# Kernel optimization log

Measured on AMD Instinct MI355X. Metric: run time of the kernel, lower is better.

Reference implementation:

```python
import jax, jax.numpy as jnp
import numpy as np

N_SRC = 50000
N_DST = 50000
N_EDGES = 1600000
BATCH = 64


def setup_inputs() -> dict:
    key = jax.random.key(0)
    k1, k2, k3, k4, k5 = jax.random.split(key, 5)
    x = jax.random.normal(k1, (BATCH, N_SRC), dtype=jnp.float32)
    # per-edge scalar weights, init like Synapse.init_weight: U(-v, v), v = sqrt(1/fan_in)~sqrt(1/32)
    v = float(np.sqrt(1.0 / 32.0))
    k = jax.random.uniform(k2, (N_EDGES,), dtype=jnp.float32, minval=-v, maxval=v)
    b = jax.random.normal(k3, (N_DST,), dtype=jnp.float32) * 0.1
    edge_src = jax.random.randint(k4, (N_EDGES,), 0, N_SRC, dtype=jnp.int32)
    edge_dst = jax.random.randint(k5, (N_EDGES,), 0, N_DST, dtype=jnp.int32)
    return {"x": x, "k": k, "b": b, "edge_src": edge_src, "edge_dst": edge_dst}


def reference(x, k, b, edge_src, edge_dst):
    # Synapse: out_e = k_e * source_output  (source output is x[:, src(e)], shape [batch])
    # msgs: [n_edges, batch]
    msgs = x.T[edge_src] * k[:, None]
    # DestinationNeuron: sum of dendrite outputs per destination + bias
    agg = jax.ops.segment_sum(msgs, edge_dst, num_segments=N_DST)  # [n_dst, batch]
    out = jax.nn.relu(agg.T + b[None, :])  # [batch, n_dst]
    return out
```

## Files before the change

### kernel.cpp

```cpp
#include <hip/hip_runtime.h>
#include <hip/hip_bf16.h>
#include <stdint.h>

#define N_SRC 50000
#define N_DST 50000
#define N_EDGES 1600000
#define BATCH 64

#define DPB 32
#define NBUCK ((N_DST + DPB - 1) / DPB)
#define CAPB 1344
#define EPB 6400
#define PTHREADS 1024
#define GTHREADS 512
#define NT ((EPB + PTHREADS - 1) / PTHREADS)

__global__ void transpose_kernel(const float* __restrict__ x,
                                 __hip_bfloat16* __restrict__ xTb,
                                 int* __restrict__ gcur) {
    __shared__ float tile[64][65];
    const int s0 = blockIdx.x * 64;
    const int tid = threadIdx.x;

    if (gcur && tid < 2) {
        const int i = blockIdx.x * 2 + tid;
        if (i < NBUCK) gcur[i] = 0;
    }

#pragma unroll
    for (int it = 0; it < 16; ++it) {
        const int i = it * 256 + tid;
        const int bi = i >> 6;
        const int sc = i & 63;
        const int s = s0 + sc;
        float v = 0.0f;
        if (s < N_SRC) v = x[(size_t)bi * N_SRC + s];
        tile[bi][sc] = v;
    }
    __syncthreads();
#pragma unroll
    for (int it = 0; it < 16; ++it) {
        const int i = it * 256 + tid;
        const int sc = i >> 6;
        const int bi = i & 63;
        const int s = s0 + sc;
        if (s < N_SRC) xTb[(size_t)s * 64 + bi] = __float2bfloat16(tile[bi][sc]);
    }
}

__global__ __launch_bounds__(PTHREADS) void partition_kernel(
        const float* __restrict__ k,
        const int* __restrict__ esrc,
        const int* __restrict__ edst,
        int* __restrict__ gcur,
        uint64_t* __restrict__ part) {
    __shared__ int bcnt[NBUCK];
    __shared__ int bcur[NBUCK];
    const int e0 = blockIdx.x * EPB;
    const int n = min(EPB, N_EDGES - e0);

    for (int i = threadIdx.x; i < NBUCK; i += PTHREADS) bcnt[i] = 0;
    __syncthreads();

    int dreg[NT];
#pragma unroll
    for (int t = 0; t < NT; ++t) {
        const int i = t * PTHREADS + threadIdx.x;
        dreg[t] = (i < n) ? edst[e0 + i] : -1;
        if (dreg[t] >= 0) atomicAdd(&bcnt[dreg[t] >> 5], 1);
    }
    __syncthreads();

    for (int bi = threadIdx.x; bi < NBUCK; bi += PTHREADS) {
        const int c = bcnt[bi];
        bcur[bi] = c ? atomicAdd(&gcur[bi], c) : 0;
    }
    __syncthreads();

#pragma unroll
    for (int t = 0; t < NT; ++t) {
        const int i = t * PTHREADS + threadIdx.x;
        if (dreg[t] >= 0) {
            const int e = e0 + i;
            const int d = dreg[t];
            const int bkt = d >> 5;
            const int slot = atomicAdd(&bcur[bkt], 1);
            if (slot < CAPB) {
                const uint32_t lo = (uint32_t)esrc[e] | ((uint32_t)(d & 31) << 16);
                part[(size_t)bkt * CAPB + slot] =
                    (uint64_t)lo | ((uint64_t)__float_as_uint(k[e]) << 32);
            }
        }
    }
}

__global__ __launch_bounds__(GTHREADS, 8) void gather_kernel(
        const __hip_bfloat16* __restrict__ xTb,
        const int* __restrict__ gcur,
        const uint64_t* __restrict__ part,
        const float* __restrict__ b,
        float* __restrict__ out) {
    __shared__ uint64_t raw[CAPB];
    __shared__ uint64_t sorted[CAPB];
    __shared__ int dbase[DPB + 1];
    __shared__ int dcur[DPB];

    const uint2* __restrict__ xTu2 = (const uint2*)xTb;

    const int bk = blockIdx.x;
    const size_t base = (size_t)bk * CAPB;
    const int n = min(gcur[bk], CAPB);
    const int d0 = bk * DPB;
    const int tid = threadIdx.x;
    const int wid = tid >> 6;
    const int lane = tid & 63;
    const int rp = lane >> 4;
    const int m = lane & 15;

    if (tid < DPB) dcur[tid] = 0;
    __syncthreads();

    for (int i = tid; i < n; i += GTHREADS) {
        const uint64_t r = part[base + i];
        raw[i] = r;
        atomicAdd(&dcur[(int)((r >> 16) & 31)], 1);
    }
    __syncthreads();

    if (wid == 0) {
        const int orig = (lane < DPB) ? dcur[lane] : 0;
        int v = orig;
#pragma unroll
        for (int d = 1; d < DPB; d <<= 1) {
            const int t = __shfl_up(v, d, 64);
            if (lane >= d) v += t;
        }
        if (lane < DPB) dbase[lane] = v - orig;
        if (lane == DPB - 1) dbase[DPB] = v;
    }
    __syncthreads();
    if (tid < DPB) dcur[tid] = dbase[tid];
    __syncthreads();

    for (int i = tid; i < n; i += GTHREADS) {
        const uint64_t r = raw[i];
        const int p = atomicAdd(&dcur[(int)((r >> 16) & 31)], 1);
        sorted[p] = r;
    }
    __syncthreads();

    float acc[4][4];
    const int dlo = wid * 4;
#pragma unroll
    for (int q = 0; q < 4; ++q) {
        const int dl = dlo + q;
        float a0 = 0.0f, a1 = 0.0f, a2 = 0.0f, a3 = 0.0f;
        int j = dbase[dl];
        const int je = dbase[dl + 1];
        for (; j + 8 <= je; j += 8) {
            const uint64_t r0 = sorted[j + rp];
            const uint64_t r1 = sorted[j + 4 + rp];
            const uint2 x0 = xTu2[(size_t)((uint32_t)r0 & 0xFFFFu) * 16 + m];
            const uint2 x1 = xTu2[(size_t)((uint32_t)r1 & 0xFFFFu) * 16 + m];
            const float k0 = __uint_as_float((uint32_t)(r0 >> 32));
            const float k1 = __uint_as_float((uint32_t)(r1 >> 32));
            a0 = fmaf(k0, __uint_as_float(x0.x << 16), a0);
            a1 = fmaf(k0, __uint_as_float(x0.x & 0xFFFF0000u), a1);
            a2 = fmaf(k0, __uint_as_float(x0.y << 16), a2);
            a3 = fmaf(k0, __uint_as_float(x0.y & 0xFFFF0000u), a3);
            a0 = fmaf(k1, __uint_as_float(x1.x << 16), a0);
            a1 = fmaf(k1, __uint_as_float(x1.x & 0xFFFF0000u), a1);
            a2 = fmaf(k1, __uint_as_float(x1.y << 16), a2);
            a3 = fmaf(k1, __uint_as_float(x1.y & 0xFFFF0000u), a3);
        }
        for (; j < je; j += 4) {
            const int idx = j + rp;
            const bool v = idx < je;
            const uint64_t r = sorted[v ? idx : j];
            const float kv = v ? __uint_as_float((uint32_t)(r >> 32)) : 0.0f;
            const uint2 xv = xTu2[(size_t)((uint32_t)r & 0xFFFFu) * 16 + m];
            a0 = fmaf(kv, __uint_as_float(xv.x << 16), a0);
            a1 = fmaf(kv, __uint_as_float(xv.x & 0xFFFF0000u), a1);
            a2 = fmaf(kv, __uint_as_float(xv.y << 16), a2);
            a3 = fmaf(kv, __uint_as_float(xv.y & 0xFFFF0000u), a3);
        }
        a0 += __shfl_xor(a0, 16); a0 += __shfl_xor(a0, 32);
        a1 += __shfl_xor(a1, 16); a1 += __shfl_xor(a1, 32);
        a2 += __shfl_xor(a2, 16); a2 += __shfl_xor(a2, 32);
        a3 += __shfl_xor(a3, 16); a3 += __shfl_xor(a3, 32);
        acc[q][0] = a0; acc[q][1] = a1; acc[q][2] = a2; acc[q][3] = a3;
    }
    __syncthreads();

    float* stg = (float*)sorted;
    if (rp == 0) {
#pragma unroll
        for (int q = 0; q < 4; ++q) {
            const int dl = dlo + q;
            stg[dl * 65 + 4 * m + 0] = acc[q][0];
            stg[dl * 65 + 4 * m + 1] = acc[q][1];
            stg[dl * 65 + 4 * m + 2] = acc[q][2];
            stg[dl * 65 + 4 * m + 3] = acc[q][3];
        }
    }
    __syncthreads();

    for (int i = tid; i < 64 * DPB; i += GTHREADS) {
        const int dl = i & (DPB - 1);
        const int bi = i >> 5;
        const int d = d0 + dl;
        if (d < N_DST)
            out[(size_t)bi * N_DST + d] = fmaxf(stg[dl * 65 + bi] + b[d], 0.0f);
    }
}

__global__ void scatter_kernel(const __hip_bfloat16* __restrict__ xTb,
                               const float* __restrict__ k,
                               const int* __restrict__ esrc,
                               const int* __restrict__ edst,
                               float* __restrict__ agg) {
    const int gtid = blockIdx.x * blockDim.x + threadIdx.x;
    const int wid = gtid >> 6;
    const int lane = threadIdx.x & 63;
    const int nwaves = (gridDim.x * blockDim.x) >> 6;
    for (int e = wid; e < N_EDGES; e += nwaves) {
        atomicAdd(&agg[(size_t)edst[e] * 64 + lane],
                  k[e] * __bfloat162float(xTb[(size_t)esrc[e] * 64 + lane]));
    }
}

__global__ void finish_kernel(const float* __restrict__ agg,
                              const float* __restrict__ b,
                              float* __restrict__ out) {
    __shared__ float tile[64 * 65];
    const int d0 = blockIdx.x * 64;
    const int tid = threadIdx.x;
#pragma unroll
    for (int it = 0; it < 16; ++it) {
        const int i = it * 256 + tid;
        const int dl = i >> 6;
        const int bi = i & 63;
        const int d = d0 + dl;
        float v = 0.0f;
        if (d < N_DST) v = agg[(size_t)d * 64 + bi];
        tile[bi * 65 + dl] = v;
    }
    __syncthreads();
#pragma unroll
    for (int it = 0; it < 16; ++it) {
        const int i = it * 256 + tid;
        const int bi = i >> 6;
        const int dl = i & 63;
        const int d = d0 + dl;
        if (d < N_DST)
            out[(size_t)bi * N_DST + d] = fmaxf(tile[bi * 65 + dl] + b[d], 0.0f);
    }
}

extern "C" void kernel_launch(void* const* d_in, const int* in_sizes, int n_in,
                              void* d_out, int out_size, void* d_ws, size_t ws_size,
                              hipStream_t stream) {
    const float* x    = (const float*)d_in[0];
    const float* k    = (const float*)d_in[1];
    const float* b    = (const float*)d_in[2];
    const int*   esrc = (const int*)d_in[3];
    const int*   edst = (const int*)d_in[4];
    float* out = (float*)d_out;

    const size_t xt_bytes   = (size_t)N_SRC * 64 * sizeof(__hip_bfloat16);
    const size_t part_bytes = (size_t)NBUCK * CAPB * sizeof(uint64_t);
    const size_t off_gcur   = xt_bytes + part_bytes;
    const size_t need_new   = off_gcur + ((NBUCK * 4 + 4095) & ~4095ull);

    __hip_bfloat16* xTb = (__hip_bfloat16*)d_ws;
    const int nblk_t = (N_SRC + 63) / 64;

    if (ws_size >= need_new) {
        uint64_t* part = (uint64_t*)((char*)d_ws + xt_bytes);
        int* gcur      = (int*)((char*)d_ws + off_gcur);

        transpose_kernel<<<nblk_t, 256, 0, stream>>>(x, xTb, gcur);
        const int nblk_p = (N_EDGES + EPB - 1) / EPB;
        partition_kernel<<<nblk_p, PTHREADS, 0, stream>>>(k, esrc, edst,
                                                          gcur, part);
        gather_kernel<<<NBUCK, GTHREADS, 0, stream>>>(xTb, gcur, part, b, out);
    } else {
        transpose_kernel<<<nblk_t, 256, 0, stream>>>(x, xTb, nullptr);
        float* agg = (float*)((char*)d_ws + ((xt_bytes + 255) & ~255ull));
        hipMemsetAsync(agg, 0, (size_t)N_DST * 64 * sizeof(float), stream);
        scatter_kernel<<<2048, 256, 0, stream>>>(xTb, k, esrc, edst, agg);
        const int nblk_f = (N_DST + 63) / 64;
        finish_kernel<<<nblk_f, 256, 0, stream>>>(agg, b, out);
    }
}
```

Measured before the change: 71.39 us.

## Fuse transpose and edge partition into one heterogeneous-block launch

Merges the x transpose and the edge bucket-partition kernels into a single launch where the first blocks partition edges and the remaining blocks transpose x to bf16. The gcur zeroing moves from the transpose kernel to a hipMemsetAsync before the launch. The aim is to overlap the two independent stages and drop one kernel boundary. In exchange, the transpose blocks now run at 1024 threads and carry the partition kernel's large shared-memory allocation, which may lower occupancy, and the added memset node brings its own overhead.

```diff
diff --git a/kernel.cpp b/kernel.cpp
--- a/kernel.cpp
+++ b/kernel.cpp
@@ -11,44 +11,15 @@
 #define NBUCK ((N_DST + DPB - 1) / DPB)
 #define CAPB 1344
 #define EPB 6400
+#define PBLOCKS ((N_EDGES + EPB - 1) / EPB)
+#define TBLOCKS ((N_SRC + 63) / 64)
 #define PTHREADS 1024
 #define GTHREADS 512
 #define NT ((EPB + PTHREADS - 1) / PTHREADS)
 
-__global__ void transpose_kernel(const float* __restrict__ x,
-                                 __hip_bfloat16* __restrict__ xTb,
-                                 int* __restrict__ gcur) {
-    __shared__ float tile[64][65];
-    const int s0 = blockIdx.x * 64;
-    const int tid = threadIdx.x;
-
-    if (gcur && tid < 2) {
-        const int i = blockIdx.x * 2 + tid;
-        if (i < NBUCK) gcur[i] = 0;
-    }
-
-#pragma unroll
-    for (int it = 0; it < 16; ++it) {
-        const int i = it * 256 + tid;
-        const int bi = i >> 6;
-        const int sc = i & 63;
-        const int s = s0 + sc;
-        float v = 0.0f;
-        if (s < N_SRC) v = x[(size_t)bi * N_SRC + s];
-        tile[bi][sc] = v;
-    }
-    __syncthreads();
-#pragma unroll
-    for (int it = 0; it < 16; ++it) {
-        const int i = it * 256 + tid;
-        const int sc = i >> 6;
-        const int bi = i & 63;
-        const int s = s0 + sc;
-        if (s < N_SRC) xTb[(size_t)s * 64 + bi] = __float2bfloat16(tile[bi][sc]);
-    }
-}
-
-__global__ __launch_bounds__(PTHREADS) void partition_kernel(
+__global__ __launch_bounds__(PTHREADS) void fused_tp_kernel(
+        const float* __restrict__ x,
+        __hip_bfloat16* __restrict__ xTb,
         const float* __restrict__ k,
         const int* __restrict__ esrc,
         const int* __restrict__ edst,
@@ -56,40 +27,69 @@
         uint64_t* __restrict__ part) {
     __shared__ int bcnt[NBUCK];
     __shared__ int bcur[NBUCK];
-    const int e0 = blockIdx.x * EPB;
-    const int n = min(EPB, N_EDGES - e0);
-
-    for (int i = threadIdx.x; i < NBUCK; i += PTHREADS) bcnt[i] = 0;
-    __syncthreads();
-
-    int dreg[NT];
-#pragma unroll
-    for (int t = 0; t < NT; ++t) {
-        const int i = t * PTHREADS + threadIdx.x;
-        dreg[t] = (i < n) ? edst[e0 + i] : -1;
-        if (dreg[t] >= 0) atomicAdd(&bcnt[dreg[t] >> 5], 1);
-    }
-    __syncthreads();
-
-    for (int bi = threadIdx.x; bi < NBUCK; bi += PTHREADS) {
-        const int c = bcnt[bi];
-        bcur[bi] = c ? atomicAdd(&gcur[bi], c) : 0;
-    }
-    __syncthreads();
-
-#pragma unroll
-    for (int t = 0; t < NT; ++t) {
-        const int i = t * PTHREADS + threadIdx.x;
-        if (dreg[t] >= 0) {
-            const int e = e0 + i;
-            const int d = dreg[t];
-            const int bkt = d >> 5;
-            const int slot = atomicAdd(&bcur[bkt], 1);
-            if (slot < CAPB) {
-                const uint32_t lo = (uint32_t)esrc[e] | ((uint32_t)(d & 31) << 16);
-                part[(size_t)bkt * CAPB + slot] =
-                    (uint64_t)lo | ((uint64_t)__float_as_uint(k[e]) << 32);
+    __shared__ float tile[64][65];
+
+    if (blockIdx.x < PBLOCKS) {
+        const int e0 = blockIdx.x * EPB;
+        const int n = min(EPB, N_EDGES - e0);
+
+        for (int i = threadIdx.x; i < NBUCK; i += PTHREADS) bcnt[i] = 0;
+        __syncthreads();
+
+        int dreg[NT];
+#pragma unroll
+        for (int t = 0; t < NT; ++t) {
+            const int i = t * PTHREADS + threadIdx.x;
+            dreg[t] = (i < n) ? edst[e0 + i] : -1;
+            if (dreg[t] >= 0) atomicAdd(&bcnt[dreg[t] >> 5], 1);
+        }
+        __syncthreads();
+
+        for (int bi = threadIdx.x; bi < NBUCK; bi += PTHREADS) {
+            const int c = bcnt[bi];
+            bcur[bi] = c ? atomicAdd(&gcur[bi], c) : 0;
+        }
+        __syncthreads();
+
+#pragma unroll
+        for (int t = 0; t < NT; ++t) {
+            const int i = t * PTHREADS + threadIdx.x;
+            if (dreg[t] >= 0) {
+                const int e = e0 + i;
+                const int d = dreg[t];
+                const int bkt = d >> 5;
+                const int slot = atomicAdd(&bcur[bkt], 1);
+                if (slot < CAPB) {
+                    const uint32_t lo = (uint32_t)esrc[e] |
+                                        ((uint32_t)(d & 31) << 16);
+                    part[(size_t)bkt * CAPB + slot] =
+                        (uint64_t)lo | ((uint64_t)__float_as_uint(k[e]) << 32);
+                }
             }
+        }
+    } else {
+        const int s0 = (blockIdx.x - PBLOCKS) * 64;
+        const int tid = threadIdx.x;
+
+#pragma unroll
+        for (int it = 0; it < 4; ++it) {
+            const int i = it * 1024 + tid;
+            const int bi = i >> 6;
+            const int sc = i & 63;
+            const int s = s0 + sc;
+            float v = 0.0f;
+            if (s < N_SRC) v = x[(size_t)bi * N_SRC + s];
+            tile[bi][sc] = v;
+        }
+        __syncthreads();
+#pragma unroll
+        for (int it = 0; it < 4; ++it) {
+            const int i = it * 1024 + tid;
+            const int sc = i >> 6;
+            const int bi = i & 63;
+            const int s = s0 + sc;
+            if (s < N_SRC)
+                xTb[(size_t)s * 64 + bi] = __float2bfloat16(tile[bi][sc]);
         }
     }
 }
@@ -214,6 +214,32 @@
     }
 }
 
+__global__ void transpose_only_kernel(const float* __restrict__ x,
+                                      __hip_bfloat16* __restrict__ xTb) {
+    __shared__ float tile[64][65];
+    const int s0 = blockIdx.x * 64;
+    const int tid = threadIdx.x;
+#pragma unroll
+    for (int it = 0; it < 16; ++it) {
+        const int i = it * 256 + tid;
+        const int bi = i >> 6;
+        const int sc = i & 63;
+        const int s = s0 + sc;
+        float v = 0.0f;
+        if (s < N_SRC) v = x[(size_t)bi * N_SRC + s];
+        tile[bi][sc] = v;
+    }
+    __syncthreads();
+#pragma unroll
+    for (int it = 0; it < 16; ++it) {
+        const int i = it * 256 + tid;
+        const int sc = i >> 6;
+        const int bi = i & 63;
+        const int s = s0 + sc;
+        if (s < N_SRC) xTb[(size_t)s * 64 + bi] = __float2bfloat16(tile[bi][sc]);
+    }
+}
+
 __global__ void scatter_kernel(const __hip_bfloat16* __restrict__ xTb,
                                const float* __restrict__ k,
                                const int* __restrict__ esrc,
@@ -273,19 +299,17 @@
     const size_t need_new   = off_gcur + ((NBUCK * 4 + 4095) & ~4095ull);
 
     __hip_bfloat16* xTb = (__hip_bfloat16*)d_ws;
-    const int nblk_t = (N_SRC + 63) / 64;
 
     if (ws_size >= need_new) {
         uint64_t* part = (uint64_t*)((char*)d_ws + xt_bytes);
         int* gcur      = (int*)((char*)d_ws + off_gcur);
 
-        transpose_kernel<<<nblk_t, 256, 0, stream>>>(x, xTb, gcur);
-        const int nblk_p = (N_EDGES + EPB - 1) / EPB;
-        partition_kernel<<<nblk_p, PTHREADS, 0, stream>>>(k, esrc, edst,
-                                                          gcur, part);
+        hipMemsetAsync(gcur, 0, NBUCK * sizeof(int), stream);
+        fused_tp_kernel<<<PBLOCKS + TBLOCKS, PTHREADS, 0, stream>>>(
+            x, xTb, k, esrc, edst, gcur, part);
         gather_kernel<<<NBUCK, GTHREADS, 0, stream>>>(xTb, gcur, part, b, out);
     } else {
-        transpose_kernel<<<nblk_t, 256, 0, stream>>>(x, xTb, nullptr);
+        transpose_only_kernel<<<TBLOCKS, 256, 0, stream>>>(x, xTb);
         float* agg = (float*)((char*)d_ws + ((xt_bytes + 255) & ~255ull));
         hipMemsetAsync(agg, 0, (size_t)N_DST * 64 * sizeof(float), stream);
         scatter_kernel<<<2048, 256, 0, stream>>>(xTb, k, esrc, edst, agg);
```

After: 69.97 us. 1.02x faster.
